# Kernel optimization log

Hardware: AMD Instinct MI355X
Metric: run time of the kernel (lower is better)

## Reference

```python
import jax, jax.numpy as jnp
import numpy as np

B, W, M, H, L, C, LR, RD = 128, 64, 512, 64, 2, 4, 16, 32
D = L * H  # concatenated GRU hidden dim


def setup_inputs() -> dict:
    key = jax.random.key(0)
    ks = jax.random.split(key, 22)
    def rn(k, shape, s=0.1):
        return jax.random.normal(k, shape, jnp.float32) * s
    return dict(
        x=jax.random.normal(ks[0], (B, W, M), jnp.float32),
        H_init=rn(ks[1], (L, M, H)),
        major_graph=rn(ks[2], (M, M), 0.05),
        wx0=rn(ks[3], (3 * H, 1)), wh0=rn(ks[4], (3 * H, H)),
        bx0=rn(ks[5], (3 * H,)), bh0=rn(ks[6], (3 * H,)),
        wx1=rn(ks[7], (3 * H, H)), wh1=rn(ks[8], (3 * H, H)),
        bx1=rn(ks[9], (3 * H,)), bh1=rn(ks[10], (3 * H,)),
        A_v=rn(ks[11], (C, LR, M)), A_g=1.0 + rn(ks[12], (C, LR)), A_b=rn(ks[13], (C, LR)),
        B_v=rn(ks[14], (C, M, LR)), B_g=1.0 + rn(ks[15], (C, M)), B_b=rn(ks[16], (C, M)),
        C_v=rn(ks[17], (C, RD, D)), C_g=1.0 + rn(ks[18], (C, RD)), C_b=rn(ks[19], (C, RD)),
        FR_w=rn(ks[20], (C, M, RD)), FR_b=rn(ks[21], (C, M)),
    )


def _wn(v, g):
    # weight_norm: W = g * v / ||v|| per output row (norm over input dim)
    return g[..., None] * v / jnp.linalg.norm(v, axis=-1, keepdims=True)


def _gru(x, h, wx, wh, bx, bh):
    gx = x @ wx.T + bx            # [B, M, 3H]
    gh = h @ wh.T + bh            # [B, M, 3H]
    xr, xz, xn = jnp.split(gx, 3, axis=-1)
    hr, hz, hn = jnp.split(gh, 3, axis=-1)
    r = jax.nn.sigmoid(xr + hr)
    z = jax.nn.sigmoid(xz + hz)
    n = jnp.tanh(xn + r * hn)
    return n + z * (h - n)


def reference(x, H_init, major_graph, wx0, wh0, bx0, bh0, wx1, wh1, bx1, bh1,
              A_v, A_g, A_b, B_v, B_g, B_b, C_v, C_g, C_b, FR_w, FR_b):
    Bsz = x.shape[0]
    Aw = _wn(A_v, A_g)            # [C, LR, M]
    Bw = _wn(B_v, B_g)            # [C, M, LR]
    Cw = _wn(C_v, C_g)            # [C, RD, D]
    # h0: [L, B, M, H]
    h0 = jnp.broadcast_to(H_init[:, None], (H_init.shape[0], Bsz) + H_init.shape[1:])
    h0_1 = h0[1]

    def step(hn, x_t):
        # NOTE: faithfully, layer0 receives the top layer's hidden from the
        # previous step; layer1 always uses the fixed h0[1].
        h1 = _gru(x_t[..., None], hn, wx0, wh0, bx0, bh0)   # [B, M, H]
        h2 = _gru(h1, h0_1, wx1, wh1, bx1, bh1)             # [B, M, H]
        x_p = jnp.swapaxes(jnp.concatenate([h1, h2], axis=-1), 1, 2)  # [B, D, M]
        x_p0 = jax.nn.relu(x_p @ major_graph)               # [B, D, M]
        a = jnp.einsum('bdm,clm->bcdl', x_p, Aw) + A_b[:, None, :]      # [B,C,D,LR]
        bmid = jnp.einsum('bcdl,cml->bcdm', a, Bw) + B_b[:, None, :]    # [B,C,D,M]
        xr = jax.nn.relu(bmid + x_p0[:, None])              # [B, C, D, M]
        xt = jnp.swapaxes(xr, 2, 3)                         # [B, C, M, D]
        y = jax.nn.sigmoid(jnp.einsum('bcmd,crd->bcmr', xt, Cw) + C_b[:, None, :])
        out = jnp.einsum('bcmr,cmr->bcm', y, FR_w) + FR_b   # [B, C, M]
        return h2, out

    _, outs = jax.lax.scan(step, h0[0], jnp.moveaxis(x, 1, 0))  # [W, B, C, M]
    final = jnp.transpose(outs, (2, 1, 0, 3))                   # [C, B, W, M]
    return final.reshape((-1,) + final.shape[2:])               # [C*B, W, M]
```

## Files before the change

kernel.cpp:

```cpp
#include <hip/hip_runtime.h>
#include <hip/hip_bf16.h>

constexpr int kB  = 128;
constexpr int kW  = 64;
constexpr int kM  = 512;
constexpr int kH  = 64;
constexpr int kC  = 4;
constexpr int kLR = 16;
constexpr int kRD = 32;
constexpr int kD  = 128;
constexpr int kNC = kB * kM;
constexpr int kN  = kM + kC * kLR;

typedef __attribute__((ext_vector_type(8))) short bf16x8;
typedef __attribute__((ext_vector_type(4))) float f32x4;

__device__ __forceinline__ float sigmf(float v) { return 1.f / (1.f + __expf(-v)); }
__device__ __forceinline__ float tanhf2(float v) { float e = __expf(2.f * v); return 1.f - 2.f / (e + 1.f); }

__device__ __forceinline__ unsigned short f2bfu(float f) {
    union { __hip_bfloat16 h; unsigned short u; } cv; cv.h = __float2bfloat16(f); return cv.u;
}
__device__ __forceinline__ float bfu2f(unsigned short s) {
    return __uint_as_float(((unsigned)s) << 16);
}

__device__ __forceinline__ void gl_lds16(const void* g, void* s) {
    __builtin_amdgcn_global_load_lds(
        (const __attribute__((address_space(1))) void*)(g),
        (__attribute__((address_space(3))) void*)(s), 16, 0, 0);
}


__global__ void k_initHc(const float* __restrict__ Hini, __hip_bfloat16* __restrict__ HcG) {
    int id = blockIdx.x * 256 + threadIdx.x;
    int cell = id >> 6, j = id & 63;
    int m = cell & (kM - 1);
    HcG[id] = __float2bfloat16(Hini[m * kH + j]);
}

__global__ void k_h1b(const float* __restrict__ Hini, __hip_bfloat16* __restrict__ H1b) {
    int id = blockIdx.x * 256 + threadIdx.x;
    H1b[id] = __float2bfloat16(Hini[(kM + (id >> 6)) * kH + (id & 63)]);
}

__global__ void k_gh1T(const float* __restrict__ Hini, const float* __restrict__ wh1,
                       const float* __restrict__ bh1, float* __restrict__ gh1T) {
    int id = blockIdx.x * 256 + threadIdx.x;
    int k = id >> 9, m = id & (kM - 1);
    float acc = bh1[k];
    #pragma unroll
    for (int j = 0; j < kH; j++)
        acc = fmaf(Hini[(kM + m) * kH + j], wh1[k * kH + j], acc);
    gh1T[id] = acc;
}

__global__ void k_packW(const float* __restrict__ wh0, const float* __restrict__ wx1,
                        __hip_bfloat16* __restrict__ W0g, __hip_bfloat16* __restrict__ W1x) {
    int id = blockIdx.x * 256 + threadIdx.x;
    W0g[id] = __float2bfloat16(wh0[id]);
    W1x[id] = __float2bfloat16(wx1[id]);
}

__global__ void k_buildGT(const float* __restrict__ G, __hip_bfloat16* __restrict__ BT) {
    int id = blockIdx.x * 256 + threadIdx.x;
    int n = id >> 9, k = id & (kM - 1);
    BT[n * kM + k] = __float2bfloat16(G[k * kM + n]);
}

__global__ void k_norm_aw(const float* __restrict__ Av, const float* __restrict__ Ag,
                          __hip_bfloat16* __restrict__ BT) {
    int row = blockIdx.x;
    int lane = threadIdx.x;
    float v[8]; float s = 0.f;
    #pragma unroll
    for (int q = 0; q < 8; q++) { v[q] = Av[row * kM + q * 64 + lane]; s += v[q] * v[q]; }
    #pragma unroll
    for (int off = 32; off > 0; off >>= 1) s += __shfl_down(s, off);
    s = __shfl(s, 0);
    float scale = Ag[row] / sqrtf(s);
    #pragma unroll
    for (int q = 0; q < 8; q++)
        BT[(kM + row) * kM + q * 64 + lane] = __float2bfloat16(v[q] * scale);
}

__global__ void k_norm_bw(const float* __restrict__ Bv, const float* __restrict__ Bg,
                          const float* __restrict__ Bb, __hip_bfloat16* __restrict__ BwNh) {
    int row = blockIdx.x * 256 + threadIdx.x;
    float v[16]; float s = 0.f;
    #pragma unroll
    for (int l = 0; l < 16; l++) { v[l] = Bv[row * 16 + l]; s += v[l] * v[l]; }
    float scale = Bg[row] / sqrtf(s);
    #pragma unroll
    for (int l = 0; l < 16; l++) BwNh[row * 32 + l] = __float2bfloat16(v[l] * scale);
    BwNh[row * 32 + 16] = __float2bfloat16(Bb[row]);
    #pragma unroll
    for (int l = 17; l < 32; l++) BwNh[row * 32 + l] = __float2bfloat16(0.f);
}

__global__ void k_norm_cw(const float* __restrict__ Cv, const float* __restrict__ Cg,
                          __hip_bfloat16* __restrict__ CwB) {
    int row = blockIdx.x;
    int lane = threadIdx.x;
    float v0 = Cv[row * kD + lane], v1 = Cv[row * kD + 64 + lane];
    float s = v0 * v0 + v1 * v1;
    #pragma unroll
    for (int off = 32; off > 0; off >>= 1) s += __shfl_down(s, off);
    s = __shfl(s, 0);
    float scale = Cg[row] / sqrtf(s);
    CwB[row * kD + lane] = __float2bfloat16(v0 * scale);
    CwB[row * kD + 64 + lane] = __float2bfloat16(v1 * scale);
}

__global__ __launch_bounds__(512) void k_gru(
    const float* __restrict__ x,
    __hip_bfloat16* __restrict__ HcG,
    const __hip_bfloat16* __restrict__ H1b,
    const __hip_bfloat16* __restrict__ W0g,
    const __hip_bfloat16* __restrict__ W1x,
    const float* __restrict__ gh1T,
    const float* __restrict__ wx0, const float* __restrict__ bx0,
    const float* __restrict__ bh0, const float* __restrict__ bx1,
    __hip_bfloat16* __restrict__ XPT, int t)
{
    __shared__ __align__(16) short W0s[192 * 64];
    __shared__ __align__(16) short W1s[192 * 64];
    __shared__ __align__(16) short HlS[128 * 64];
    __shared__ float xsh[128];

    const int tid = threadIdx.x;
    const int w = tid >> 6, lane = tid & 63;
    const int lr = lane & 15, lq = lane >> 4;
    const int b = blockIdx.x;
    const int mBlk = blockIdx.y * 128;
    const unsigned short* HcU = (const unsigned short*)HcG;
    const unsigned short* H1U = (const unsigned short*)H1b;
    const size_t cellBase = (size_t)b * kM + mBlk;

    #pragma unroll
    for (int it = 0; it < 3; it++) {
        int cid = it * 512 + tid; int row = cid >> 3, c = cid & 7;
        gl_lds16(W0g + row * 64 + ((c ^ (row & 7)) * 8), W0s + cid * 8);
    }
    #pragma unroll
    for (int it = 0; it < 3; it++) {
        int cid = it * 512 + tid; int row = cid >> 3, c = cid & 7;
        gl_lds16(W1x + row * 64 + ((c ^ (row & 7)) * 8), W1s + cid * 8);
    }
    if (tid < 128) xsh[tid] = x[((size_t)b * kW + t) * kM + mBlk + tid];
    __syncthreads();

    const int cl = w * 16 + lr;

    bf16x8 a0[2];
    a0[0] = *(const bf16x8*)&HcU[(cellBase + cl) * 64 + lq * 8];
    a0[1] = *(const bf16x8*)&HcU[(cellBase + cl) * 64 + (4 + lq) * 8];
    f32x4 aR[4] = {}, aZ[4] = {}, aN[4] = {};
    #pragma unroll
    for (int kc = 0; kc < 2; kc++) {
        #pragma unroll
        for (int gt = 0; gt < 4; gt++) {
            const int gR = gt * 16 + lr;
            const int gZ = 64 + gt * 16 + lr;
            const int gN = 128 + gt * 16 + lr;
            bf16x8 bR = *(const bf16x8*)&W0s[gR * 64 + (((kc * 4 + lq) ^ (gR & 7)) * 8)];
            bf16x8 bZ = *(const bf16x8*)&W0s[gZ * 64 + (((kc * 4 + lq) ^ (gZ & 7)) * 8)];
            bf16x8 bN = *(const bf16x8*)&W0s[gN * 64 + (((kc * 4 + lq) ^ (gN & 7)) * 8)];
            aR[gt] = __builtin_amdgcn_mfma_f32_16x16x32_bf16(a0[kc], bR, aR[gt], 0, 0, 0);
            aZ[gt] = __builtin_amdgcn_mfma_f32_16x16x32_bf16(a0[kc], bZ, aZ[gt], 0, 0, 0);
            aN[gt] = __builtin_amdgcn_mfma_f32_16x16x32_bf16(a0[kc], bN, aN[gt], 0, 0, 0);
        }
    }

    #pragma unroll
    for (int gt = 0; gt < 4; gt++) {
        const int i = gt * 16 + lr;
        const float wxr = wx0[i], wxz = wx0[64 + i], wxn = wx0[128 + i];
        const float bsr = bx0[i] + bh0[i];
        const float bsz = bx0[64 + i] + bh0[64 + i];
        const float bxn = bx0[128 + i], bhn = bh0[128 + i];
        unsigned short hu[4];
        #pragma unroll
        for (int r2 = 0; r2 < 4; r2++) {
            const int clr = w * 16 + lq * 4 + r2;
            const float xv = xsh[clr];
            float rr = sigmf(aR[gt][r2] + bsr + xv * wxr);
            float zz = sigmf(aZ[gt][r2] + bsz + xv * wxz);
            float nn = tanhf2(bxn + xv * wxn + rr * (aN[gt][r2] + bhn));
            float hp = bfu2f(HcU[(cellBase + clr) * 64 + i]);
            float h1 = nn + zz * (hp - nn);
            unsigned short u = f2bfu(h1);
            HlS[clr * 64 + (((i >> 3) ^ (clr & 7)) * 8) + (i & 7)] = (short)u;
            hu[r2] = u;
        }
        ushort4 pk; pk.x = hu[0]; pk.y = hu[1]; pk.z = hu[2]; pk.w = hu[3];
        *(ushort4*)((unsigned short*)XPT + (size_t)(b * 128 + i) * kM + mBlk + w * 16 + lq * 4) = pk;
    }

    bf16x8 a1[2];
    a1[0] = *(const bf16x8*)&HlS[cl * 64 + ((lq ^ (cl & 7)) * 8)];
    a1[1] = *(const bf16x8*)&HlS[cl * 64 + (((4 + lq) ^ (cl & 7)) * 8)];
    f32x4 cR[4] = {}, cZ[4] = {}, cN[4] = {};
    #pragma unroll
    for (int kc = 0; kc < 2; kc++) {
        #pragma unroll
        for (int gt = 0; gt < 4; gt++) {
            const int gR = gt * 16 + lr;
            const int gZ = 64 + gt * 16 + lr;
            const int gN = 128 + gt * 16 + lr;
            bf16x8 bR = *(const bf16x8*)&W1s[gR * 64 + (((kc * 4 + lq) ^ (gR & 7)) * 8)];
            bf16x8 bZ = *(const bf16x8*)&W1s[gZ * 64 + (((kc * 4 + lq) ^ (gZ & 7)) * 8)];
            bf16x8 bN = *(const bf16x8*)&W1s[gN * 64 + (((kc * 4 + lq) ^ (gN & 7)) * 8)];
            cR[gt] = __builtin_amdgcn_mfma_f32_16x16x32_bf16(a1[kc], bR, cR[gt], 0, 0, 0);
            cZ[gt] = __builtin_amdgcn_mfma_f32_16x16x32_bf16(a1[kc], bZ, cZ[gt], 0, 0, 0);
            cN[gt] = __builtin_amdgcn_mfma_f32_16x16x32_bf16(a1[kc], bN, cN[gt], 0, 0, 0);
        }
    }

    const int mb4 = mBlk + w * 16 + lq * 4;
    #pragma unroll
    for (int gt = 0; gt < 4; gt++) {
        const int i = gt * 16 + lr;
        const float bxr = bx1[i], bxz = bx1[64 + i], bxn = bx1[128 + i];
        f32x4 gr4 = *(const f32x4*)&gh1T[(size_t)i * kM + mb4];
        f32x4 gz4 = *(const f32x4*)&gh1T[(size_t)(64 + i) * kM + mb4];
        f32x4 gn4 = *(const f32x4*)&gh1T[(size_t)(128 + i) * kM + mb4];
        unsigned short hu[4];
        #pragma unroll
        for (int r2 = 0; r2 < 4; r2++) {
            const int clr = w * 16 + lq * 4 + r2;
            float rr = sigmf(cR[gt][r2] + bxr + gr4[r2]);
            float zz = sigmf(cZ[gt][r2] + bxz + gz4[r2]);
            float nn = tanhf2(cN[gt][r2] + bxn + rr * gn4[r2]);
            float h01 = bfu2f(H1U[(size_t)(mBlk + clr) * 64 + i]);
            float h2 = nn + zz * (h01 - nn);
            unsigned short u = f2bfu(h2);
            hu[r2] = u;
            ((unsigned short*)HcG)[(cellBase + clr) * 64 + i] = u;
        }
        ushort4 pk; pk.x = hu[0]; pk.y = hu[1]; pk.z = hu[2]; pk.w = hu[3];
        *(ushort4*)((unsigned short*)XPT + (size_t)(b * 128 + 64 + i) * kM + mBlk + w * 16 + lq * 4) = pk;
    }
}

__global__ __launch_bounds__(512, 4) void k_tail(
    const __hip_bfloat16* __restrict__ X,
    const __hip_bfloat16* __restrict__ BT,
    const float* __restrict__ Ab,
    const __hip_bfloat16* __restrict__ BwNh,
    const __hip_bfloat16* __restrict__ CwB,
    const float* __restrict__ Cb, const float* __restrict__ FRw,
    const float* __restrict__ FRb, float* __restrict__ OUT, int t)
{
    __shared__ __align__(16) short SM[40960];
    short* xp0L = SM;
    short* aL   = SM + 16384;
    short* Xr   = SM + 24576;

    const int tid = threadIdx.x;
    const int b = blockIdx.x, mseg = blockIdx.y;
    const int w = tid >> 6, lane = tid & 63;
    const int lr = lane & 15, lq = lane >> 4;
    const int wm = w >> 2, wn = w & 3;

    f32x4 acc[4][3] = {};
    const __hip_bfloat16* Xb = X + (size_t)b * 128 * kM;

    auto STAGE = [&](int kk, int buf) {
        short* AsB = SM + buf * 20480;
        short* BsB = AsB + 8192;
        #pragma unroll
        for (int it = 0; it < 2; it++) {
            int cid = it * 512 + tid;
            int row = cid >> 3, ch = cid & 7;
            int cg = ch ^ (row & 7);
            gl_lds16(Xb + (size_t)row * kM + kk + cg * 8, AsB + cid * 8);
        }
        #pragma unroll
        for (int it = 0; it < 3; it++) {
            int cid = it * 512 + tid;
            int j = cid >> 3, ch = cid & 7;
            int cg = ch ^ (j & 7);
            int n = (j < 128) ? (mseg * 128 + j) : (384 + j);
            gl_lds16(BT + (size_t)n * kM + kk + cg * 8, BsB + cid * 8);
        }
    };

    STAGE(0, 0);
    __syncthreads();

    int cur = 0;
    for (int ki = 0; ki < 8; ki++) {
        if (ki < 7) STAGE((ki + 1) * 64, cur ^ 1);
        const short* AsB = SM + cur * 20480;
        const short* BsB = AsB + 8192;
        #pragma unroll
        for (int w2 = 0; w2 < 2; w2++) {
            bf16x8 af[4], bfr[3];
            #pragma unroll
            for (int fi = 0; fi < 4; fi++) {
                int row = wm * 64 + fi * 16 + lr;
                af[fi] = *(const bf16x8*)&AsB[row * 64 + (((w2 * 4 + lq) ^ (row & 7)) * 8)];
            }
            #pragma unroll
            for (int fj = 0; fj < 3; fj++) {
                int col = wn * 48 + fj * 16 + lr;
                bfr[fj] = *(const bf16x8*)&BsB[col * 64 + (((w2 * 4 + lq) ^ (col & 7)) * 8)];
            }
            #pragma unroll
            for (int fi = 0; fi < 4; fi++)
                #pragma unroll
                for (int fj = 0; fj < 3; fj++)
                    acc[fi][fj] = __builtin_amdgcn_mfma_f32_16x16x32_bf16(
                        af[fi], bfr[fj], acc[fi][fj], 0, 0, 0);
        }
        __syncthreads();
        cur ^= 1;
    }

    #pragma unroll
    for (int fj = 0; fj < 3; fj++) {
        const int colg = wn * 48 + fj * 16 + lr;
        if (colg < 128) {
            #pragma unroll
            for (int fi = 0; fi < 4; fi++) {
                const int d0 = wm * 64 + fi * 16 + lq * 4;
                const int c16 = d0 >> 3, half = lq & 1;
                unsigned lo = (unsigned)f2bfu(fmaxf(acc[fi][fj][0], 0.f)) |
                              ((unsigned)f2bfu(fmaxf(acc[fi][fj][1], 0.f)) << 16);
                unsigned hi = (unsigned)f2bfu(fmaxf(acc[fi][fj][2], 0.f)) |
                              ((unsigned)f2bfu(fmaxf(acc[fi][fj][3], 0.f)) << 16);
                uint2 pk; pk.x = lo; pk.y = hi;
                *(uint2*)&xp0L[colg * 128 + ((c16 ^ (colg & 7)) * 8) + half * 4] = pk;
            }
        } else {
            const int clc = colg - 128;
            const float ab = Ab[clc];
            #pragma unroll
            for (int fi = 0; fi < 4; fi++) {
                #pragma unroll
                for (int r = 0; r < 4; r++) {
                    const int d = wm * 64 + fi * 16 + lq * 4 + r;
                    aL[d * 64 + (((clc >> 3) ^ (d & 7)) * 8) + (clc & 7)] =
                        (short)f2bfu(acc[fi][fj][r] + ab);
                }
            }
        }
    }
    __syncthreads();

    const int c = w & 3;
    const int mhalf = w >> 2;
    bf16x8 af2[8];
    #pragma unroll
    for (int dt = 0; dt < 8; dt++) {
        bf16x8 v = {};
        const int d = dt * 16 + lr;
        if (lq < 2) {
            v = *(const bf16x8*)&aL[d * 64 + (((c * 2 + lq) ^ (d & 7)) * 8)];
        } else if (lq == 2) {
            v[0] = (short)0x3F80;
        }
        af2[dt] = v;
    }
    bf16x8 cwf[2][4];
    #pragma unroll
    for (int rt = 0; rt < 2; rt++)
        #pragma unroll
        for (int s = 0; s < 4; s++)
            cwf[rt][s] = *(const bf16x8*)&CwB[((size_t)(c * kRD + rt * 16 + lr)) * kD + s * 32 + lq * 8];
    const float cbv0 = Cb[c * kRD + lr];
    const float cbv1 = Cb[c * kRD + 16 + lr];
    short* Xrw = Xr + w * 2048;

    for (int mt = 0; mt < 4; mt++) {
        const int mg = mseg * 128 + mhalf * 64 + mt * 16 + lr;
        bf16x8 bf1 = *(const bf16x8*)&BwNh[((size_t)c * kM + mg) * 32 + lq * 8];
        f32x4 acc1[8] = {};
        #pragma unroll
        for (int dt = 0; dt < 8; dt++)
            acc1[dt] = __builtin_amdgcn_mfma_f32_16x16x32_bf16(af2[dt], bf1, acc1[dt], 0, 0, 0);

        const int mlT = mhalf * 64 + mt * 16 + lr;
        #pragma unroll
        for (int dt = 0; dt < 8; dt++) {
            const int c16 = dt * 2 + (lq >> 1), half = lq & 1;
            uint2 xv = *(const uint2*)&xp0L[mlT * 128 + ((c16 ^ (mlT & 7)) * 8) + half * 4];
            float x0 = bfu2f((unsigned short)(xv.x & 0xFFFF));
            float x1 = bfu2f((unsigned short)(xv.x >> 16));
            float x2 = bfu2f((unsigned short)(xv.y & 0xFFFF));
            float x3 = bfu2f((unsigned short)(xv.y >> 16));
            unsigned lo = (unsigned)f2bfu(fmaxf(acc1[dt][0] + x0, 0.f)) |
                          ((unsigned)f2bfu(fmaxf(acc1[dt][1] + x1, 0.f)) << 16);
            unsigned hi = (unsigned)f2bfu(fmaxf(acc1[dt][2] + x2, 0.f)) |
                          ((unsigned)f2bfu(fmaxf(acc1[dt][3] + x3, 0.f)) << 16);
            uint2 pk; pk.x = lo; pk.y = hi;
            *(uint2*)&Xrw[lr * 128 + ((c16 ^ (lr & 7)) * 8) + half * 4] = pk;
        }

        bf16x8 xa[4];
        #pragma unroll
        for (int s = 0; s < 4; s++)
            xa[s] = *(const bf16x8*)&Xrw[lr * 128 + (((s * 4 + lq) ^ (lr & 7)) * 8)];
        float po0 = 0.f, po1 = 0.f, po2 = 0.f, po3 = 0.f;
        const int mrow = mseg * 128 + mhalf * 64 + mt * 16 + lq * 4;
        #pragma unroll
        for (int rt = 0; rt < 2; rt++) {
            f32x4 a2 = {};
            #pragma unroll
            for (int s = 0; s < 4; s++)
                a2 = __builtin_amdgcn_mfma_f32_16x16x32_bf16(xa[s], cwf[rt][s], a2, 0, 0, 0);
            const float cb = rt ? cbv1 : cbv0;
            const int r = rt * 16 + lr;
            po0 = fmaf(sigmf(a2[0] + cb), FRw[((size_t)c * kM + mrow + 0) * kRD + r], po0);
            po1 = fmaf(sigmf(a2[1] + cb), FRw[((size_t)c * kM + mrow + 1) * kRD + r], po1);
            po2 = fmaf(sigmf(a2[2] + cb), FRw[((size_t)c * kM + mrow + 2) * kRD + r], po2);
            po3 = fmaf(sigmf(a2[3] + cb), FRw[((size_t)c * kM + mrow + 3) * kRD + r], po3);
        }
        #pragma unroll
        for (int off = 8; off > 0; off >>= 1) {
            po0 += __shfl_xor(po0, off);
            po1 += __shfl_xor(po1, off);
            po2 += __shfl_xor(po2, off);
            po3 += __shfl_xor(po3, off);
        }
        if (lr == 0) {
            const float* frb = &FRb[c * kM + mrow];
            float4 o;
            o.x = po0 + frb[0]; o.y = po1 + frb[1];
            o.z = po2 + frb[2]; o.w = po3 + frb[3];
            *(float4*)&OUT[((size_t)(c * kB + b) * kW + t) * kM + mrow] = o;
        }
    }
}

extern "C" void kernel_launch(void* const* d_in, const int* in_sizes, int n_in,
                              void* d_out, int out_size, void* d_ws, size_t ws_size,
                              hipStream_t stream) {
    const float* x    = (const float*)d_in[0];
    const float* Hini = (const float*)d_in[1];
    const float* G    = (const float*)d_in[2];
    const float* wx0  = (const float*)d_in[3];
    const float* wh0  = (const float*)d_in[4];
    const float* bx0  = (const float*)d_in[5];
    const float* bh0  = (const float*)d_in[6];
    const float* wx1  = (const float*)d_in[7];
    const float* wh1  = (const float*)d_in[8];
    const float* bx1  = (const float*)d_in[9];
    const float* bh1  = (const float*)d_in[10];
    const float* A_v  = (const float*)d_in[11];
    const float* A_g  = (const float*)d_in[12];
    const float* A_b  = (const float*)d_in[13];
    const float* B_v  = (const float*)d_in[14];
    const float* B_g  = (const float*)d_in[15];
    const float* B_b  = (const float*)d_in[16];
    const float* C_v  = (const float*)d_in[17];
    const float* C_g  = (const float*)d_in[18];
    const float* C_b  = (const float*)d_in[19];
    const float* FR_w = (const float*)d_in[20];
    const float* FR_b = (const float*)d_in[21];
    float* out = (float*)d_out;

    char* w = (char*)d_ws;
    __hip_bfloat16* HcG  = (__hip_bfloat16*)w; w += (size_t)kNC * 64 * 2;
    __hip_bfloat16* XPT  = (__hip_bfloat16*)w; w += (size_t)128 * kNC * 2;
    __hip_bfloat16* BT   = (__hip_bfloat16*)w; w += (size_t)kN * kM * 2;
    __hip_bfloat16* H1b  = (__hip_bfloat16*)w; w += (size_t)kM * kH * 2;
    __hip_bfloat16* W0g  = (__hip_bfloat16*)w; w += (size_t)192 * 64 * 2;
    __hip_bfloat16* W1xg = (__hip_bfloat16*)w; w += (size_t)192 * 64 * 2;
    float*          gh1T = (float*)w;          w += (size_t)192 * kM * 4;
    __hip_bfloat16* BwNh = (__hip_bfloat16*)w; w += (size_t)2048 * 32 * 2;
    __hip_bfloat16* CwB  = (__hip_bfloat16*)w; w += (size_t)kC * kRD * kD * 2;

    k_initHc<<<16384, 256, 0, stream>>>(Hini, HcG);
    k_h1b<<<128, 256, 0, stream>>>(Hini, H1b);
    k_gh1T<<<384, 256, 0, stream>>>(Hini, wh1, bh1, gh1T);
    k_packW<<<48, 256, 0, stream>>>(wh0, wx1, W0g, W1xg);
    k_buildGT<<<1024, 256, 0, stream>>>(G, BT);
    k_norm_aw<<<64, 64, 0, stream>>>(A_v, A_g, BT);
    k_norm_bw<<<8, 256, 0, stream>>>(B_v, B_g, B_b, BwNh);
    k_norm_cw<<<128, 64, 0, stream>>>(C_v, C_g, CwB);

    for (int t = 0; t < kW; t++) {
        k_gru<<<dim3(128, 4), 512, 0, stream>>>(x, HcG, H1b, W0g, W1xg, gh1T,
                                                wx0, bx0, bh0, bx1, XPT, t);
        k_tail<<<dim3(128, 4), 512, 0, stream>>>(XPT, BT, A_b, BwNh, CwB,
                                                 C_b, FR_w, FR_b, out, t);
    }
}
```

Before: 3.146 ms.

## Fuse GRU step t+1 with tail step t in one launch using double-buffered XPT

Merges the GRU recurrence for step t+1 and the tail projection for step t into a single kernel whose blocks alternate between the two roles. XPT is double-buffered so the tail reads step t while the GRU writes step t+1, halving the launch count and letting the two stages overlap on the GPU. The tail's K-loop also swaps __syncthreads for explicit vmcnt waits plus s_barrier to pipeline its global-to-LDS loads. Risks: the fused kernel uses the tail's launch bounds and shared memory for GRU blocks, which may change occupancy and register pressure.

```diff
diff --git a/kernel.cpp b/kernel.cpp
--- a/kernel.cpp
+++ b/kernel.cpp
@@ -112,7 +112,9 @@
     CwB[row * kD + 64 + lane] = __float2bfloat16(v1 * scale);
 }
 
-__global__ __launch_bounds__(512) void k_gru(
+__device__ __forceinline__ void gru_body(
+    short* W0s, short* W1s, short* HlS, float* xsh,
+    int b, int mBlk,
     const float* __restrict__ x,
     __hip_bfloat16* __restrict__ HcG,
     const __hip_bfloat16* __restrict__ H1b,
@@ -123,16 +125,9 @@
     const float* __restrict__ bh0, const float* __restrict__ bx1,
     __hip_bfloat16* __restrict__ XPT, int t)
 {
-    __shared__ __align__(16) short W0s[192 * 64];
-    __shared__ __align__(16) short W1s[192 * 64];
-    __shared__ __align__(16) short HlS[128 * 64];
-    __shared__ float xsh[128];
-
     const int tid = threadIdx.x;
     const int w = tid >> 6, lane = tid & 63;
     const int lr = lane & 15, lq = lane >> 4;
-    const int b = blockIdx.x;
-    const int mBlk = blockIdx.y * 128;
     const unsigned short* HcU = (const unsigned short*)HcG;
     const unsigned short* H1U = (const unsigned short*)H1b;
     const size_t cellBase = (size_t)b * kM + mBlk;
@@ -243,22 +238,19 @@
     }
 }
 
-__global__ __launch_bounds__(512, 4) void k_tail(
-    const __hip_bfloat16* __restrict__ X,
-    const __hip_bfloat16* __restrict__ BT,
-    const float* __restrict__ Ab,
-    const __hip_bfloat16* __restrict__ BwNh,
-    const __hip_bfloat16* __restrict__ CwB,
-    const float* __restrict__ Cb, const float* __restrict__ FRw,
-    const float* __restrict__ FRb, float* __restrict__ OUT, int t)
+__device__ __forceinline__ void tail_body(
+    short* SM, int b, int mseg,
+    const __hip_bfloat16* __restrict__ X, const __hip_bfloat16* __restrict__ BT,
+    const float* __restrict__ Ab, const __hip_bfloat16* __restrict__ BwNh,
+    const __hip_bfloat16* __restrict__ CwB, const float* __restrict__ Cb,
+    const float* __restrict__ FRw, const float* __restrict__ FRb,
+    float* __restrict__ OUT, int t)
 {
-    __shared__ __align__(16) short SM[40960];
     short* xp0L = SM;
     short* aL   = SM + 16384;
     short* Xr   = SM + 24576;
 
     const int tid = threadIdx.x;
-    const int b = blockIdx.x, mseg = blockIdx.y;
     const int w = tid >> 6, lane = tid & 63;
     const int lr = lane & 15, lq = lane >> 4;
     const int wm = w >> 2, wn = w & 3;
@@ -287,11 +279,16 @@
     };
 
     STAGE(0, 0);
-    __syncthreads();
-
     int cur = 0;
     for (int ki = 0; ki < 8; ki++) {
-        if (ki < 7) STAGE((ki + 1) * 64, cur ^ 1);
+        if (ki < 7) {
+            STAGE((ki + 1) * 64, cur ^ 1);
+            asm volatile("s_waitcnt vmcnt(5)" ::: "memory");
+        } else {
+            asm volatile("s_waitcnt vmcnt(0)" ::: "memory");
+        }
+        __builtin_amdgcn_sched_barrier(0);
+        __builtin_amdgcn_s_barrier();
         const short* AsB = SM + cur * 20480;
         const short* BsB = AsB + 8192;
         #pragma unroll
@@ -314,7 +311,7 @@
                     acc[fi][fj] = __builtin_amdgcn_mfma_f32_16x16x32_bf16(
                         af[fi], bfr[fj], acc[fi][fj], 0, 0, 0);
         }
-        __syncthreads();
+        __builtin_amdgcn_s_barrier();
         cur ^= 1;
     }
 
@@ -434,6 +431,46 @@
     }
 }
 
+__global__ __launch_bounds__(512) void k_gru(
+    const float* __restrict__ x, __hip_bfloat16* __restrict__ HcG,
+    const __hip_bfloat16* __restrict__ H1b, const __hip_bfloat16* __restrict__ W0g,
+    const __hip_bfloat16* __restrict__ W1x, const float* __restrict__ gh1T,
+    const float* __restrict__ wx0, const float* __restrict__ bx0,
+    const float* __restrict__ bh0, const float* __restrict__ bx1,
+    __hip_bfloat16* __restrict__ XPT, int t)
+{
+    __shared__ __align__(16) short SMg[33024];
+    gru_body(SMg, SMg + 12288, SMg + 24576, (float*)(SMg + 32768),
+             blockIdx.x, blockIdx.y * 128,
+             x, HcG, H1b, W0g, W1x, gh1T, wx0, bx0, bh0, bx1, XPT, t);
+}
+
+__global__ __launch_bounds__(512, 4) void k_step(
+    const float* __restrict__ x, __hip_bfloat16* __restrict__ HcG,
+    const __hip_bfloat16* __restrict__ H1b, const __hip_bfloat16* __restrict__ W0g,
+    const __hip_bfloat16* __restrict__ W1x, const float* __restrict__ gh1T,
+    const float* __restrict__ wx0, const float* __restrict__ bx0,
+    const float* __restrict__ bh0, const float* __restrict__ bx1,
+    const __hip_bfloat16* __restrict__ XPTr, __hip_bfloat16* __restrict__ XPTw,
+    const __hip_bfloat16* __restrict__ BT, const float* __restrict__ Ab,
+    const __hip_bfloat16* __restrict__ BwNh, const __hip_bfloat16* __restrict__ CwB,
+    const float* __restrict__ Cb, const float* __restrict__ FRw,
+    const float* __restrict__ FRb, float* __restrict__ OUT,
+    int t, int do_gru)
+{
+    __shared__ __align__(16) short SM[40960];
+    const int id2 = blockIdx.x >> 1;
+    const int b = id2 & 127, seg = id2 >> 7;
+    if (blockIdx.x & 1) {
+        if (!do_gru) return;
+        gru_body(SM, SM + 12288, SM + 24576, (float*)(SM + 32768),
+                 b, seg * 128,
+                 x, HcG, H1b, W0g, W1x, gh1T, wx0, bx0, bh0, bx1, XPTw, t + 1);
+    } else {
+        tail_body(SM, b, seg, XPTr, BT, Ab, BwNh, CwB, Cb, FRw, FRb, OUT, t);
+    }
+}
+
 extern "C" void kernel_launch(void* const* d_in, const int* in_sizes, int n_in,
                               void* d_out, int out_size, void* d_ws, size_t ws_size,
                               hipStream_t stream) {
@@ -463,7 +500,8 @@
 
     char* w = (char*)d_ws;
     __hip_bfloat16* HcG  = (__hip_bfloat16*)w; w += (size_t)kNC * 64 * 2;
-    __hip_bfloat16* XPT  = (__hip_bfloat16*)w; w += (size_t)128 * kNC * 2;
+    __hip_bfloat16* XPT0 = (__hip_bfloat16*)w; w += (size_t)128 * kNC * 2;
+    __hip_bfloat16* XPT1 = (__hip_bfloat16*)w; w += (size_t)128 * kNC * 2;
     __hip_bfloat16* BT   = (__hip_bfloat16*)w; w += (size_t)kN * kM * 2;
     __hip_bfloat16* H1b  = (__hip_bfloat16*)w; w += (size_t)kM * kH * 2;
     __hip_bfloat16* W0g  = (__hip_bfloat16*)w; w += (size_t)192 * 64 * 2;
@@ -471,6 +509,7 @@
     float*          gh1T = (float*)w;          w += (size_t)192 * kM * 4;
     __hip_bfloat16* BwNh = (__hip_bfloat16*)w; w += (size_t)2048 * 32 * 2;
     __hip_bfloat16* CwB  = (__hip_bfloat16*)w; w += (size_t)kC * kRD * kD * 2;
+    __hip_bfloat16* XPTs[2] = {XPT0, XPT1};
 
     k_initHc<<<16384, 256, 0, stream>>>(Hini, HcG);
     k_h1b<<<128, 256, 0, stream>>>(Hini, H1b);
@@ -481,10 +520,13 @@
     k_norm_bw<<<8, 256, 0, stream>>>(B_v, B_g, B_b, BwNh);
     k_norm_cw<<<128, 64, 0, stream>>>(C_v, C_g, CwB);
 
+    k_gru<<<dim3(128, 4), 512, 0, stream>>>(x, HcG, H1b, W0g, W1xg, gh1T,
+                                            wx0, bx0, bh0, bx1, XPTs[0], 0);
     for (int t = 0; t < kW; t++) {
-        k_gru<<<dim3(128, 4), 512, 0, stream>>>(x, HcG, H1b, W0g, W1xg, gh1T,
-                                                wx0, bx0, bh0, bx1, XPT, t);
-        k_tail<<<dim3(128, 4), 512, 0, stream>>>(XPT, BT, A_b, BwNh, CwB,
-                                                 C_b, FR_w, FR_b, out, t);
-    }
-}
+        k_step<<<1024, 512, 0, stream>>>(x, HcG, H1b, W0g, W1xg, gh1T,
+                                         wx0, bx0, bh0, bx1,
+                                         XPTs[t & 1], XPTs[(t + 1) & 1],
+                                         BT, A_b, BwNh, CwB, C_b, FR_w, FR_b, out,
+                                         t, (t + 1 < kW) ? 1 : 0);
+    }
+}
```

New measurement: 3.428 ms. 9.0% more time.
